# Optimization experiments

Measured on AMD Instinct MI355X. Metric: run time of the kernel, lower is better.

The kernel has to match this reference:

```python
import jax, jax.numpy as jnp
import numpy as np

IN_DIM = 8192
OUT_DIM = 4096
LAMB = 2.0      # lamb
ALPHA = 0.001   # heb_lr
GAMMA = 0.99    # gamma


def setup_inputs() -> dict:
    key = jax.random.key(0)
    k1, k2 = jax.random.split(key)
    x = jax.random.normal(k1, (IN_DIM,), dtype=jnp.float32)
    # fc.weight initialized uniform(0, 1), shape [out, in], no bias
    W = jax.random.uniform(k2, (OUT_DIM, IN_DIM), dtype=jnp.float32)
    exp_avg = jnp.zeros((OUT_DIM,), dtype=jnp.float32)
    return {"x": x, "W": W, "exp_avg": exp_avg}


def reference(x, W, exp_avg):
    # --- fc (no bias) ---
    pre = W @ x                                  # [out]
    # --- inhibition: relu, then power-normalize by max^lamb ---
    r = jax.nn.relu(pre)
    max_pow = jnp.abs(jnp.max(r)) ** LAMB        # max taken via .item() in torch
    y = (r ** LAMB) / max_pow                    # [out]
    # --- Hebbian weight update ---
    # torch: A = einsum('jk,lkm,m->lj', W.T, itensors, y) where itensors[l] is a
    # padded (l+1)-identity => A[l,j] = sum_{k<=l} W[k,j]*y[k], i.e. a cumsum
    # over the output axis. Then A *= y[:, None].
    outer = y[:, None] * x[None, :]              # [out, in]
    A = jnp.cumsum(y[:, None] * W, axis=0) * y[:, None]  # [out, in]
    new_W = W + ALPHA * (outer - A)
    # --- exponential average of activities ---
    new_exp_avg = GAMMA * exp_avg + (1.0 - GAMMA) * y
    return (y, new_W, new_exp_avg)
```

## Files before the change

### kernel.cpp

```cpp
#include <hip/hip_runtime.h>
#include <hip/hip_bf16.h>

#define IN_DIM 8192
#define OUT_DIM 4096
#define CHUNKS 256
#define RPB 16
#define IN4 (IN_DIM / 4)

constexpr float ALPHA = 0.001f;
constexpr float GAMMA = 0.99f;

__global__ __launch_bounds__(1024)
void k1_matvec_partials(const float* __restrict__ x,
                        const float* __restrict__ W,
                        float* __restrict__ r2buf,
                        float* __restrict__ chunkmax,
                        float* __restrict__ q)
{
    __shared__ float sx[IN_DIM];
    __shared__ float red[16];

    const int t = threadIdx.x;
    const int c = blockIdx.x;
    const int lane = t & 63;
    const int wid = t >> 6;

    float4* sx4 = (float4*)sx;
    const float4* x4 = (const float4*)x;
    sx4[t] = x4[t];
    sx4[t + 1024] = x4[t + 1024];
    __syncthreads();

    const float4 xa = sx4[t];
    const float4 xb = sx4[t + 1024];

    float4 acc0 = make_float4(0.f, 0.f, 0.f, 0.f);
    float4 acc1 = make_float4(0.f, 0.f, 0.f, 0.f);
    float maxr = 0.f;

    for (int rr = 0; rr < RPB; ++rr) {
        const int row = c * RPB + rr;
        const float4* wrow4 = (const float4*)(W + (size_t)row * IN_DIM);
        const float4 w0 = wrow4[t];
        const float4 w1 = wrow4[t + 1024];

        float local = w0.x * xa.x + w0.y * xa.y + w0.z * xa.z + w0.w * xa.w
                    + w1.x * xb.x + w1.y * xb.y + w1.z * xb.z + w1.w * xb.w;

        for (int off = 32; off; off >>= 1) local += __shfl_down(local, off);
        if (lane == 0) red[wid] = local;
        __syncthreads();

        float pre = 0.f;
        #pragma unroll
        for (int i = 0; i < 16; ++i) pre += red[i];
        __syncthreads();

        const float r  = pre > 0.f ? pre : 0.f;
        const float r2 = r * r;
        maxr = fmaxf(maxr, r);
        if (t == 0) r2buf[row] = r2;

        acc0.x += r2 * w0.x; acc0.y += r2 * w0.y;
        acc0.z += r2 * w0.z; acc0.w += r2 * w0.w;
        acc1.x += r2 * w1.x; acc1.y += r2 * w1.y;
        acc1.z += r2 * w1.z; acc1.w += r2 * w1.w;
    }

    if (t == 0) chunkmax[c] = maxr;

    float4* q4 = (float4*)(q + (size_t)c * IN_DIM);
    q4[t] = acc0;
    q4[t + 1024] = acc1;
}

__global__ __launch_bounds__(1024)
void k2_y_expavg(const float* __restrict__ r2buf,
                 const float* __restrict__ chunkmax,
                 const float* __restrict__ exp_avg,
                 float* __restrict__ y_out,
                 float* __restrict__ exp_out,
                 float* __restrict__ invbuf)
{
    __shared__ float sm[16];
    const int t = threadIdx.x;
    const int lane = t & 63;
    const int wid = t >> 6;

    float v = (t < CHUNKS) ? chunkmax[t] : 0.f;
    for (int off = 32; off; off >>= 1) v = fmaxf(v, __shfl_down(v, off));
    if (lane == 0) sm[wid] = v;
    __syncthreads();
    float m = 0.f;
    #pragma unroll
    for (int i = 0; i < 16; ++i) m = fmaxf(m, sm[i]);

    const float inv = 1.f / (m * m);

    const int i = blockIdx.x * 1024 + t;
    const float yv = r2buf[i] * inv;
    y_out[i] = yv;
    exp_out[i] = GAMMA * exp_avg[i] + (1.f - GAMMA) * yv;

    if (blockIdx.x == 0 && t == 0) invbuf[0] = inv;
}

__global__ __launch_bounds__(256)
void k3_chunk_scan(float* __restrict__ q)
{
    const int j = blockIdx.x * 256 + threadIdx.x;
    float s = 0.f;
    for (int cc = 0; cc < CHUNKS; cc += 8) {
        float v[8];
        #pragma unroll
        for (int u = 0; u < 8; ++u) v[u] = q[(size_t)(cc + u) * IN_DIM + j];
        #pragma unroll
        for (int u = 0; u < 8; ++u) { const float tmp = v[u]; v[u] = s; s += tmp; }
        #pragma unroll
        for (int u = 0; u < 8; ++u) q[(size_t)(cc + u) * IN_DIM + j] = v[u];
    }
}

__global__ __launch_bounds__(256)
void k4_apply(const float* __restrict__ x,
              const float* __restrict__ W,
              const float* __restrict__ r2buf,
              const float* __restrict__ q,
              const float* __restrict__ invbuf,
              float* __restrict__ newW)
{
    __shared__ float sr2[RPB];
    __shared__ float sinv;

    const int c = blockIdx.y;
    const int tile = blockIdx.x;
    const int t = threadIdx.x;

    if (t < RPB) sr2[t] = r2buf[c * RPB + t];
    if (t == RPB) sinv = invbuf[0];
    __syncthreads();
    const float inv = sinv;

    const int j4 = tile * 256 + t;
    const float4 xv = ((const float4*)x)[j4];
    float4 s = ((const float4*)q)[(size_t)c * IN4 + j4];

    #pragma unroll
    for (int rr = 0; rr < RPB; ++rr) {
        const int row = c * RPB + rr;
        const float4 w = ((const float4*)W)[(size_t)row * IN4 + j4];
        const float r2 = sr2[rr];
        s.x += r2 * w.x; s.y += r2 * w.y; s.z += r2 * w.z; s.w += r2 * w.w;
        const float yl = inv * r2;
        const float a  = ALPHA * yl;
        float4 o;
        o.x = w.x + a * (xv.x - inv * s.x);
        o.y = w.y + a * (xv.y - inv * s.y);
        o.z = w.z + a * (xv.z - inv * s.z);
        o.w = w.w + a * (xv.w - inv * s.w);
        ((float4*)newW)[(size_t)row * IN4 + j4] = o;
    }
}

extern "C" void kernel_launch(void* const* d_in, const int* in_sizes, int n_in,
                              void* d_out, int out_size, void* d_ws, size_t ws_size,
                              hipStream_t stream)
{
    const float* x       = (const float*)d_in[0];
    const float* W       = (const float*)d_in[1];
    const float* exp_avg = (const float*)d_in[2];

    float* y_out   = (float*)d_out;
    float* newW    = (float*)d_out + OUT_DIM;
    float* exp_out = (float*)d_out + OUT_DIM + (size_t)OUT_DIM * IN_DIM;

    float* ws       = (float*)d_ws;
    float* q        = ws;
    float* r2buf    = ws + (size_t)CHUNKS * IN_DIM;
    float* chunkmax = r2buf + OUT_DIM;
    float* invbuf   = chunkmax + CHUNKS;

    k1_matvec_partials<<<CHUNKS, 1024, 0, stream>>>(x, W, r2buf, chunkmax, q);
    k2_y_expavg<<<OUT_DIM / 1024, 1024, 0, stream>>>(r2buf, chunkmax, exp_avg,
                                                     y_out, exp_out, invbuf);
    k3_chunk_scan<<<IN_DIM / 256, 256, 0, stream>>>(q);
    k4_apply<<<dim3(IN_DIM / 1024, CHUNKS), 256, 0, stream>>>(x, W, r2buf, q,
                                                              invbuf, newW);
}
```

Measured before the change: 276.8 us.

## Batch matvec row reductions, fuse y/exp-avg with segmented chunk scan, nontemporal stores

The matvec kernel now loads four W rows at a time and reduces their dot products with one barrier pair per batch instead of two per row. The y/exp_avg kernel and the column scan are merged into one kernel of 256 blocks, and each column's scan is split across 8 segments with a shared-memory offset pass, which increases parallelism and removes a launch. The apply kernel preloads all 16 W rows into registers and writes newW with nontemporal stores to cut cache pollution. Costs are higher register pressure in the apply and matvec kernels, plus a second read pass over q in the scan.

```diff
diff --git a/kernel.cpp b/kernel.cpp
--- a/kernel.cpp
+++ b/kernel.cpp
@@ -6,9 +6,16 @@
 #define CHUNKS 256
 #define RPB 16
 #define IN4 (IN_DIM / 4)
+#define BATCH 4
+
+#define SCAN_COLS 32
+#define SCAN_SEGS 8
+#define SEG_LEN (CHUNKS / SCAN_SEGS)
 
 constexpr float ALPHA = 0.001f;
 constexpr float GAMMA = 0.99f;
+
+typedef float f32x4 __attribute__((ext_vector_type(4)));
 
 __global__ __launch_bounds__(1024)
 void k1_matvec_partials(const float* __restrict__ x,
@@ -18,7 +25,8 @@
                         float* __restrict__ q)
 {
     __shared__ float sx[IN_DIM];
-    __shared__ float red[16];
+    __shared__ float red[BATCH][16];
+    __shared__ float sr2[RPB];
 
     const int t = threadIdx.x;
     const int c = blockIdx.x;
@@ -26,98 +34,129 @@
     const int wid = t >> 6;
 
     float4* sx4 = (float4*)sx;
-    const float4* x4 = (const float4*)x;
-    sx4[t] = x4[t];
-    sx4[t + 1024] = x4[t + 1024];
-    __syncthreads();
-
+    sx4[t] = ((const float4*)x)[t];
+    sx4[t + 1024] = ((const float4*)x)[t + 1024];
+    __syncthreads();
     const float4 xa = sx4[t];
     const float4 xb = sx4[t + 1024];
 
     float4 acc0 = make_float4(0.f, 0.f, 0.f, 0.f);
     float4 acc1 = make_float4(0.f, 0.f, 0.f, 0.f);
-    float maxr = 0.f;
-
-    for (int rr = 0; rr < RPB; ++rr) {
-        const int row = c * RPB + rr;
-        const float4* wrow4 = (const float4*)(W + (size_t)row * IN_DIM);
-        const float4 w0 = wrow4[t];
-        const float4 w1 = wrow4[t + 1024];
-
-        float local = w0.x * xa.x + w0.y * xa.y + w0.z * xa.z + w0.w * xa.w
-                    + w1.x * xb.x + w1.y * xb.y + w1.z * xb.z + w1.w * xb.w;
-
-        for (int off = 32; off; off >>= 1) local += __shfl_down(local, off);
-        if (lane == 0) red[wid] = local;
+
+    for (int bb = 0; bb < RPB / BATCH; ++bb) {
+        const int rb = c * RPB + bb * BATCH;
+
+        float4 w0[BATCH], w1[BATCH];
+        #pragma unroll
+        for (int r = 0; r < BATCH; ++r) {
+            const float4* row4 = (const float4*)(W + (size_t)(rb + r) * IN_DIM);
+            w0[r] = row4[t];
+            w1[r] = row4[t + 1024];
+        }
+
+        #pragma unroll
+        for (int r = 0; r < BATCH; ++r) {
+            float d = w0[r].x * xa.x + w0[r].y * xa.y + w0[r].z * xa.z + w0[r].w * xa.w
+                    + w1[r].x * xb.x + w1[r].y * xb.y + w1[r].z * xb.z + w1[r].w * xb.w;
+            for (int off = 32; off; off >>= 1) d += __shfl_down(d, off);
+            if (lane == 0) red[r][wid] = d;
+        }
         __syncthreads();
 
-        float pre = 0.f;
-        #pragma unroll
-        for (int i = 0; i < 16; ++i) pre += red[i];
+        if (wid < BATCH) {
+            float v = (lane < 16) ? red[wid][lane] : 0.f;
+            for (int off = 8; off; off >>= 1) v += __shfl_down(v, off);
+            if (lane == 0) {
+                const float rr = v > 0.f ? v : 0.f;
+                const float r2 = rr * rr;
+                sr2[bb * BATCH + wid] = r2;
+                r2buf[rb + wid] = r2;
+            }
+        }
         __syncthreads();
 
-        const float r  = pre > 0.f ? pre : 0.f;
-        const float r2 = r * r;
-        maxr = fmaxf(maxr, r);
-        if (t == 0) r2buf[row] = r2;
-
-        acc0.x += r2 * w0.x; acc0.y += r2 * w0.y;
-        acc0.z += r2 * w0.z; acc0.w += r2 * w0.w;
-        acc1.x += r2 * w1.x; acc1.y += r2 * w1.y;
-        acc1.z += r2 * w1.z; acc1.w += r2 * w1.w;
-    }
-
-    if (t == 0) chunkmax[c] = maxr;
+        #pragma unroll
+        for (int r = 0; r < BATCH; ++r) {
+            const float r2 = sr2[bb * BATCH + r];
+            acc0.x += r2 * w0[r].x; acc0.y += r2 * w0[r].y;
+            acc0.z += r2 * w0[r].z; acc0.w += r2 * w0[r].w;
+            acc1.x += r2 * w1[r].x; acc1.y += r2 * w1[r].y;
+            acc1.z += r2 * w1[r].z; acc1.w += r2 * w1[r].w;
+        }
+    }
+
+    if (t == 0) {
+        float m = 0.f;
+        #pragma unroll
+        for (int i = 0; i < RPB; ++i) m = fmaxf(m, sr2[i]);
+        chunkmax[c] = m;
+    }
 
     float4* q4 = (float4*)(q + (size_t)c * IN_DIM);
     q4[t] = acc0;
     q4[t + 1024] = acc1;
 }
 
-__global__ __launch_bounds__(1024)
-void k2_y_expavg(const float* __restrict__ r2buf,
-                 const float* __restrict__ chunkmax,
-                 const float* __restrict__ exp_avg,
-                 float* __restrict__ y_out,
-                 float* __restrict__ exp_out,
-                 float* __restrict__ invbuf)
-{
-    __shared__ float sm[16];
+__global__ __launch_bounds__(256)
+void k2_fused(const float* __restrict__ r2buf,
+              const float* __restrict__ chunkmax,
+              const float* __restrict__ exp_avg,
+              float* __restrict__ y_out,
+              float* __restrict__ exp_out,
+              float* __restrict__ invbuf,
+              float* __restrict__ q)
+{
+    __shared__ float sred[4];
+    __shared__ float sinv;
+    __shared__ float segsum[SCAN_SEGS][SCAN_COLS];
+
     const int t = threadIdx.x;
+    const int b = blockIdx.x;
     const int lane = t & 63;
     const int wid = t >> 6;
 
-    float v = (t < CHUNKS) ? chunkmax[t] : 0.f;
+    float v = chunkmax[t];
     for (int off = 32; off; off >>= 1) v = fmaxf(v, __shfl_down(v, off));
-    if (lane == 0) sm[wid] = v;
-    __syncthreads();
-    float m = 0.f;
+    if (lane == 0) sred[wid] = v;
+    __syncthreads();
+    if (t == 0) {
+        const float m = fmaxf(fmaxf(sred[0], sred[1]), fmaxf(sred[2], sred[3]));
+        sinv = 1.f / m;
+    }
+    __syncthreads();
+    const float inv = sinv;
+
+    if (t < 16) {
+        const int i = b * 16 + t;
+        const float yv = r2buf[i] * inv;
+        y_out[i] = yv;
+        exp_out[i] = GAMMA * exp_avg[i] + (1.f - GAMMA) * yv;
+    }
+    if (b == 0 && t == 0) invbuf[0] = inv;
+
+    const int col = t & (SCAN_COLS - 1);
+    const int seg = t >> 5;
+    const int j = b * SCAN_COLS + col;
+
+    float s = 0.f;
+    #pragma unroll 8
+    for (int u = 0; u < SEG_LEN; ++u)
+        s += q[(size_t)(seg * SEG_LEN + u) * IN_DIM + j];
+    segsum[seg][col] = s;
+    __syncthreads();
+
+    float off_ = 0.f;
     #pragma unroll
-    for (int i = 0; i < 16; ++i) m = fmaxf(m, sm[i]);
-
-    const float inv = 1.f / (m * m);
-
-    const int i = blockIdx.x * 1024 + t;
-    const float yv = r2buf[i] * inv;
-    y_out[i] = yv;
-    exp_out[i] = GAMMA * exp_avg[i] + (1.f - GAMMA) * yv;
-
-    if (blockIdx.x == 0 && t == 0) invbuf[0] = inv;
-}
-
-__global__ __launch_bounds__(256)
-void k3_chunk_scan(float* __restrict__ q)
-{
-    const int j = blockIdx.x * 256 + threadIdx.x;
-    float s = 0.f;
-    for (int cc = 0; cc < CHUNKS; cc += 8) {
-        float v[8];
-        #pragma unroll
-        for (int u = 0; u < 8; ++u) v[u] = q[(size_t)(cc + u) * IN_DIM + j];
-        #pragma unroll
-        for (int u = 0; u < 8; ++u) { const float tmp = v[u]; v[u] = s; s += tmp; }
-        #pragma unroll
-        for (int u = 0; u < 8; ++u) q[(size_t)(cc + u) * IN_DIM + j] = v[u];
+    for (int s2 = 0; s2 < SCAN_SEGS; ++s2)
+        if (s2 < seg) off_ += segsum[s2][col];
+
+    float run = off_;
+    #pragma unroll 8
+    for (int u = 0; u < SEG_LEN; ++u) {
+        const size_t idx = (size_t)(seg * SEG_LEN + u) * IN_DIM + j;
+        const float val = q[idx];
+        q[idx] = run;
+        run += val;
     }
 }
 
@@ -145,20 +184,23 @@
     const float4 xv = ((const float4*)x)[j4];
     float4 s = ((const float4*)q)[(size_t)c * IN4 + j4];
 
+    float4 w[RPB];
+    #pragma unroll
+    for (int rr = 0; rr < RPB; ++rr)
+        w[rr] = ((const float4*)W)[(size_t)(c * RPB + rr) * IN4 + j4];
+
     #pragma unroll
     for (int rr = 0; rr < RPB; ++rr) {
-        const int row = c * RPB + rr;
-        const float4 w = ((const float4*)W)[(size_t)row * IN4 + j4];
         const float r2 = sr2[rr];
-        s.x += r2 * w.x; s.y += r2 * w.y; s.z += r2 * w.z; s.w += r2 * w.w;
-        const float yl = inv * r2;
-        const float a  = ALPHA * yl;
-        float4 o;
-        o.x = w.x + a * (xv.x - inv * s.x);
-        o.y = w.y + a * (xv.y - inv * s.y);
-        o.z = w.z + a * (xv.z - inv * s.z);
-        o.w = w.w + a * (xv.w - inv * s.w);
-        ((float4*)newW)[(size_t)row * IN4 + j4] = o;
+        s.x += r2 * w[rr].x; s.y += r2 * w[rr].y;
+        s.z += r2 * w[rr].z; s.w += r2 * w[rr].w;
+        const float a = ALPHA * inv * r2;
+        f32x4 o;
+        o.x = w[rr].x + a * (xv.x - inv * s.x);
+        o.y = w[rr].y + a * (xv.y - inv * s.y);
+        o.z = w[rr].z + a * (xv.z - inv * s.z);
+        o.w = w[rr].w + a * (xv.w - inv * s.w);
+        __builtin_nontemporal_store(o, (f32x4*)(newW + (size_t)(c * RPB + rr) * IN_DIM) + j4);
     }
 }
 
@@ -181,9 +223,8 @@
     float* invbuf   = chunkmax + CHUNKS;
 
     k1_matvec_partials<<<CHUNKS, 1024, 0, stream>>>(x, W, r2buf, chunkmax, q);
-    k2_y_expavg<<<OUT_DIM / 1024, 1024, 0, stream>>>(r2buf, chunkmax, exp_avg,
-                                                     y_out, exp_out, invbuf);
-    k3_chunk_scan<<<IN_DIM / 256, 256, 0, stream>>>(q);
+    k2_fused<<<IN_DIM / SCAN_COLS, 256, 0, stream>>>(r2buf, chunkmax, exp_avg,
+                                                     y_out, exp_out, invbuf, q);
     k4_apply<<<dim3(IN_DIM / 1024, CHUNKS), 256, 0, stream>>>(x, W, r2buf, q,
                                                               invbuf, newW);
 }
```

Result: no change. 274.7 us (-0.7%).
